# Performance work log

Hardware: AMD Instinct MI355X
Metric: run time of the kernel (lower is better)

## Reference

```python
import jax, jax.numpy as jnp
import numpy as np

N_NODES = 50000
N_EDGES = 800000
IN_DIM = 96
HID = 96


def setup_inputs() -> dict:
    key = jax.random.key(0)
    k1, k2, k3, k4 = jax.random.split(key, 4)
    x = jax.random.normal(k1, (N_NODES, IN_DIM), dtype=jnp.float32)
    edge_index = jax.random.randint(k2, (2, N_EDGES), 0, N_NODES, dtype=jnp.int64)
    s1 = 1.0 / np.sqrt(IN_DIM)
    s2 = 1.0 / np.sqrt(HID)
    W1 = jax.random.normal(k3, (IN_DIM, HID), dtype=jnp.float32) * s1
    b1 = jnp.zeros((HID,), dtype=jnp.float32)
    W2 = jax.random.normal(k4, (HID, HID), dtype=jnp.float32) * s2
    b2 = jnp.zeros((HID,), dtype=jnp.float32)
    return {"x": x, "edge_index": edge_index, "W1": W1, "b1": b1, "W2": W2, "b2": b2}


def _gcn_conv(x, src, dst, norm, W, b, n_nodes):
    # x' = D^{-1/2}(A+I)D^{-1/2} X W + b  (PyG GCNConv semantics)
    xw = x @ W                           # [N, out]
    msg = xw[src] * norm[:, None]        # gather + edge-normalize, [E+N, out]
    agg = jax.ops.segment_sum(msg, dst, num_segments=n_nodes)  # scatter-add
    return agg + b


def reference(x, edge_index, W1, b1, W2, b2):
    n_nodes = x.shape[0]
    loops = jnp.arange(n_nodes, dtype=edge_index.dtype)
    src = jnp.concatenate([edge_index[0], loops])  # sources (j)
    dst = jnp.concatenate([edge_index[1], loops])  # targets (i), aggregation index
    # symmetric normalization with self-loops; degree counted at targets
    deg = jax.ops.segment_sum(jnp.ones(dst.shape, dtype=x.dtype), dst, num_segments=n_nodes)
    dinv = jnp.where(deg > 0, jax.lax.rsqrt(deg), 0.0)
    norm = dinv[src] * dinv[dst]
    h = jax.nn.relu(_gcn_conv(x, src, dst, norm, W1, b1, n_nodes))
    h = jax.nn.relu(_gcn_conv(h, src, dst, norm, W2, b2, n_nodes))
    return h
```

## Files before the change

### kernel.cpp

```cpp
#include <hip/hip_runtime.h>

#define N_NODES 50000
#define N_EDGES 800000
#define DIM 96
#define FEAT_ELEMS (N_NODES * DIM)
#define NBLK 196
#define EGRID 3125
#define CGRID 4688
#define WGRID 10
#define AGRID 3125
#define GGRID 782

typedef __attribute__((ext_vector_type(8))) short short8;
typedef __attribute__((ext_vector_type(4))) float float4v;

__device__ __forceinline__ float bf16_to_f32(unsigned short u) {
    unsigned int w = ((unsigned int)u) << 16;
    float f;
    __builtin_memcpy(&f, &w, 4);
    return f;
}
__device__ __forceinline__ unsigned short f32_to_bf16_rne(float f) {
    unsigned int w;
    __builtin_memcpy(&w, &f, 4);
    unsigned int r = (w + 0x7FFFu + ((w >> 16) & 1u)) >> 16;
    return (unsigned short)r;
}
__device__ __forceinline__ unsigned int pack_bf16x2(float lo, float hi) {
    return (unsigned int)f32_to_bf16_rne(lo) | ((unsigned int)f32_to_bf16_rne(hi) << 16);
}

__device__ __forceinline__ int edge_at(const void* ep, int is64, int idx) {
    if (is64) return (int)((const long long*)ep)[idx];
    return ((const int*)ep)[idx];
}

__global__ __launch_bounds__(256) void prolog_kernel(const unsigned int* edges,
                                                     const unsigned int* x,
                                                     int* flagE, int* flagF, int* cnt) {
    __shared__ unsigned int sh[256];
    int t = threadIdx.x;
    int b = blockIdx.x;
    if (b < NBLK) {
        int i = b * 256 + t;
        if (i < N_NODES) cnt[i] = 0;
        return;
    }
    if (b == NBLK) {
        if (t < 64) {
            unsigned int acc = 0;
            for (int k = 0; k < 4; ++k) {
                int idx = t * 4 + k;
                int pos = 1 + 2 * idx * 3109;
                acc |= edges[pos];
            }
            sh[t] = acc;
        }
        __syncthreads();
        if (t == 0) {
            unsigned int a = 0;
            for (int i = 0; i < 64; ++i) a |= sh[i];
            *flagE = (a == 0u) ? 1 : 0;
        }
        return;
    }
    unsigned int w = x[t * 9000];
    unsigned int e = (w >> 7) & 0xFFu;
    sh[t] = (e >= 100u && e <= 135u) ? 1u : 0u;
    __syncthreads();
    if (t == 0) {
        int c = 0;
        for (int i = 0; i < 256; ++i) c += (int)sh[i];
        *flagF = (c >= 128) ? 1 : 0;
    }
}

__global__ __launch_bounds__(256) void count_convert_kernel(const void* __restrict__ edges,
                                                            const void* __restrict__ x,
                                                            const void* __restrict__ W1,
                                                            const void* __restrict__ W2,
                                                            const int* __restrict__ flagE,
                                                            const int* __restrict__ flagF,
                                                            int* __restrict__ cnt,
                                                            unsigned short* __restrict__ srcu,
                                                            unsigned short* __restrict__ dstu,
                                                            unsigned short* __restrict__ rank,
                                                            unsigned short* __restrict__ xb,
                                                            unsigned short* __restrict__ wsw1,
                                                            unsigned short* __restrict__ wsw2) {
    int b = blockIdx.x;
    if (b < EGRID) {
        int e = b * 256 + threadIdx.x;
        int is64 = *flagE;
        int s = edge_at(edges, is64, e);
        int d = edge_at(edges, is64, N_EDGES + e);
        srcu[e] = (unsigned short)s;
        dstu[e] = (unsigned short)d;
        rank[e] = (unsigned short)atomicAdd(&cnt[d], 1);
        return;
    }
    if (b < EGRID + CGRID) {
        int i4 = ((b - EGRID) * 256 + threadIdx.x) * 4;
        if (i4 >= FEAT_ELEMS) return;
        int isbf16 = *flagF;
        ushort4 o;
        if (isbf16) {
            o = *(const ushort4*)((const unsigned short*)x + i4);
        } else {
            float4 v = *(const float4*)((const float*)x + i4);
            o.x = f32_to_bf16_rne(v.x);
            o.y = f32_to_bf16_rne(v.y);
            o.z = f32_to_bf16_rne(v.z);
            o.w = f32_to_bf16_rne(v.w);
        }
        *(ushort4*)(xb + i4) = o;
        return;
    }
    int wi = b - EGRID - CGRID;
    int which = wi / 5;
    int f = (wi - which * 5) * 256 + threadIdx.x;
    if (f >= 1152) return;
    const void* Wp = which ? W2 : W1;
    unsigned short* Op = which ? wsw2 : wsw1;
    int wBf16 = *flagF;
    int kt = f / 384;
    int rem = f - kt * 384;
    int nt = rem >> 6;
    int ln64 = rem & 63;
    int q = ln64 >> 4, ln = ln64 & 15;
    int k0 = kt * 32 + q * 8;
    int n = nt * 16 + ln;
    unsigned short e[8];
    if (wBf16) {
        const unsigned short* Wh = (const unsigned short*)Wp;
        #pragma unroll
        for (int j = 0; j < 8; ++j) e[j] = Wh[(k0 + j) * DIM + n];
    } else {
        const float* Wf = (const float*)Wp;
        #pragma unroll
        for (int j = 0; j < 8; ++j) e[j] = f32_to_bf16_rne(Wf[(k0 + j) * DIM + n]);
    }
    uint4 pk;
    pk.x = (unsigned int)e[0] | ((unsigned int)e[1] << 16);
    pk.y = (unsigned int)e[2] | ((unsigned int)e[3] << 16);
    pk.z = (unsigned int)e[4] | ((unsigned int)e[5] << 16);
    pk.w = (unsigned int)e[6] | ((unsigned int)e[7] << 16);
    *(uint4*)&Op[f * 8] = pk;
}

__global__ __launch_bounds__(256) void scan_blocksum_kernel(const int* cnt, int* blockSums) {
    __shared__ int sh[256];
    int i = blockIdx.x * 256 + threadIdx.x;
    sh[threadIdx.x] = (i < N_NODES) ? cnt[i] : 0;
    __syncthreads();
    for (int off = 128; off > 0; off >>= 1) {
        if (threadIdx.x < off) sh[threadIdx.x] += sh[threadIdx.x + off];
        __syncthreads();
    }
    if (threadIdx.x == 0) blockSums[blockIdx.x] = sh[0];
}

__global__ __launch_bounds__(256) void scan_apply_kernel(const int* __restrict__ cnt,
                                                         const int* __restrict__ blockSums,
                                                         int* __restrict__ row_ptr,
                                                         float* __restrict__ dinv) {
    __shared__ int sb[256];
    __shared__ int sh[256];
    int t = threadIdx.x;
    sb[t] = (t < NBLK) ? blockSums[t] : 0;
    __syncthreads();
    for (int off = 1; off < 256; off <<= 1) {
        int u = (t >= off) ? sb[t - off] : 0;
        __syncthreads();
        sb[t] += u;
        __syncthreads();
    }
    int b = blockIdx.x;
    int blockOff = (b == 0) ? 0 : sb[b - 1];
    if (b == 0 && t == 0) row_ptr[N_NODES] = sb[NBLK - 1];

    int i = b * 256 + t;
    int c = (i < N_NODES) ? cnt[i] : 0;
    sh[t] = c;
    __syncthreads();
    for (int off = 1; off < 256; off <<= 1) {
        int u = (t >= off) ? sh[t - off] : 0;
        __syncthreads();
        sh[t] += u;
        __syncthreads();
    }
    if (i < N_NODES) {
        row_ptr[i] = sh[t] - c + blockOff;
        dinv[i]    = rsqrtf((float)(c + 1));
    }
}

__global__ __launch_bounds__(256) void fill_direct_kernel(const unsigned short* __restrict__ dstu,
                                                          const unsigned short* __restrict__ srcu,
                                                          const unsigned short* __restrict__ rank,
                                                          const int* __restrict__ row_ptr,
                                                          const float* __restrict__ dinv,
                                                          unsigned short* __restrict__ csr_src,
                                                          float* __restrict__ csr_w) {
    int e = blockIdx.x * 256 + threadIdx.x;
    if (e >= N_EDGES) return;
    int d = dstu[e];
    int s = srcu[e];
    int pos = row_ptr[d] + (int)rank[e];
    csr_src[pos] = (unsigned short)s;
    csr_w[pos]   = dinv[s] * dinv[d];
}

__global__ __launch_bounds__(256) void gather_kernel(const unsigned short* __restrict__ feat,
                                                     const int* __restrict__ row_ptr,
                                                     const unsigned short* __restrict__ csr_src,
                                                     const float* __restrict__ csr_w,
                                                     const float* __restrict__ dinv,
                                                     unsigned short* __restrict__ aggb) {
    int gid = blockIdx.x * 256 + threadIdx.x;
    int g = gid >> 4;
    int l = gid & 15;
    if (g >= N_NODES) return;
    float di = dinv[g];
    int gb = g * DIM + l * 2;
    ushort2 sv0 = *(const ushort2*)&feat[gb];
    ushort2 sv1 = *(const ushort2*)&feat[gb + 32];
    ushort2 sv2 = *(const ushort2*)&feat[gb + 64];
    float wself = di * di;
    float a0 = wself * bf16_to_f32(sv0.x), a1 = wself * bf16_to_f32(sv0.y);
    float a2 = wself * bf16_to_f32(sv1.x), a3 = wself * bf16_to_f32(sv1.y);
    float a4 = wself * bf16_to_f32(sv2.x), a5 = wself * bf16_to_f32(sv2.y);
    int e = row_ptr[g], e1 = row_ptr[g + 1];
    for (; e + 4 <= e1; e += 4) {
        int s0 = csr_src[e + 0];
        int s1 = csr_src[e + 1];
        int s2 = csr_src[e + 2];
        int s3 = csr_src[e + 3];
        float w0 = csr_w[e + 0];
        float w1 = csr_w[e + 1];
        float w2 = csr_w[e + 2];
        float w3 = csr_w[e + 3];
        int b0 = s0 * DIM + l * 2;
        int b1 = s1 * DIM + l * 2;
        int b2 = s2 * DIM + l * 2;
        int b3 = s3 * DIM + l * 2;
        ushort2 p0 = *(const ushort2*)&feat[b0];
        ushort2 p1 = *(const ushort2*)&feat[b0 + 32];
        ushort2 p2 = *(const ushort2*)&feat[b0 + 64];
        ushort2 q0 = *(const ushort2*)&feat[b1];
        ushort2 q1 = *(const ushort2*)&feat[b1 + 32];
        ushort2 q2 = *(const ushort2*)&feat[b1 + 64];
        ushort2 r0 = *(const ushort2*)&feat[b2];
        ushort2 r1 = *(const ushort2*)&feat[b2 + 32];
        ushort2 r2 = *(const ushort2*)&feat[b2 + 64];
        ushort2 t0 = *(const ushort2*)&feat[b3];
        ushort2 t1 = *(const ushort2*)&feat[b3 + 32];
        ushort2 t2 = *(const ushort2*)&feat[b3 + 64];
        a0 = fmaf(w0, bf16_to_f32(p0.x), a0);  a1 = fmaf(w0, bf16_to_f32(p0.y), a1);
        a2 = fmaf(w0, bf16_to_f32(p1.x), a2);  a3 = fmaf(w0, bf16_to_f32(p1.y), a3);
        a4 = fmaf(w0, bf16_to_f32(p2.x), a4);  a5 = fmaf(w0, bf16_to_f32(p2.y), a5);
        a0 = fmaf(w1, bf16_to_f32(q0.x), a0);  a1 = fmaf(w1, bf16_to_f32(q0.y), a1);
        a2 = fmaf(w1, bf16_to_f32(q1.x), a2);  a3 = fmaf(w1, bf16_to_f32(q1.y), a3);
        a4 = fmaf(w1, bf16_to_f32(q2.x), a4);  a5 = fmaf(w1, bf16_to_f32(q2.y), a5);
        a0 = fmaf(w2, bf16_to_f32(r0.x), a0);  a1 = fmaf(w2, bf16_to_f32(r0.y), a1);
        a2 = fmaf(w2, bf16_to_f32(r1.x), a2);  a3 = fmaf(w2, bf16_to_f32(r1.y), a3);
        a4 = fmaf(w2, bf16_to_f32(r2.x), a4);  a5 = fmaf(w2, bf16_to_f32(r2.y), a5);
        a0 = fmaf(w3, bf16_to_f32(t0.x), a0);  a1 = fmaf(w3, bf16_to_f32(t0.y), a1);
        a2 = fmaf(w3, bf16_to_f32(t1.x), a2);  a3 = fmaf(w3, bf16_to_f32(t1.y), a3);
        a4 = fmaf(w3, bf16_to_f32(t2.x), a4);  a5 = fmaf(w3, bf16_to_f32(t2.y), a5);
    }
    for (; e < e1; ++e) {
        int s = csr_src[e];
        float w = csr_w[e];
        int b0 = s * DIM + l * 2;
        ushort2 p0 = *(const ushort2*)&feat[b0];
        ushort2 p1 = *(const ushort2*)&feat[b0 + 32];
        ushort2 p2 = *(const ushort2*)&feat[b0 + 64];
        a0 = fmaf(w, bf16_to_f32(p0.x), a0);  a1 = fmaf(w, bf16_to_f32(p0.y), a1);
        a2 = fmaf(w, bf16_to_f32(p1.x), a2);  a3 = fmaf(w, bf16_to_f32(p1.y), a3);
        a4 = fmaf(w, bf16_to_f32(p2.x), a4);  a5 = fmaf(w, bf16_to_f32(p2.y), a5);
    }
    *(unsigned int*)&aggb[gb]      = pack_bf16x2(a0, a1);
    *(unsigned int*)&aggb[gb + 32] = pack_bf16x2(a2, a3);
    *(unsigned int*)&aggb[gb + 64] = pack_bf16x2(a4, a5);
}

__global__ __launch_bounds__(256) void gemm_mfma_kernel(const unsigned short* __restrict__ A,
                                                        const unsigned short* __restrict__ Wsw,
                                                        const void* __restrict__ bias,
                                                        const int* __restrict__ flagF,
                                                        void* __restrict__ out, int outMode) {
    int wBf16 = *flagF;
    int outBf16 = (outMode == 2) ? wBf16 : outMode;
    int t = threadIdx.x;
    int wave = t >> 6;
    int lane = t & 63;
    int quad = lane >> 4, ln = lane & 15;
    int m0 = blockIdx.x * 64 + wave * 16;
    int arow = m0 + ln;
    bool arowok = (arow < N_NODES);

    float4v acc[6];
    #pragma unroll
    for (int nt = 0; nt < 6; ++nt) acc[nt] = (float4v){0.f, 0.f, 0.f, 0.f};

    #pragma unroll
    for (int kt = 0; kt < 3; ++kt) {
        short8 af;
        if (arowok) {
            af = *(const short8*)&A[arow * DIM + kt * 32 + quad * 8];
        } else {
            af = (short8){0, 0, 0, 0, 0, 0, 0, 0};
        }
        #pragma unroll
        for (int nt = 0; nt < 6; ++nt) {
            short8 bf = *(const short8*)&Wsw[((kt * 6 + nt) * 64 + lane) * 8];
            acc[nt] = __builtin_amdgcn_mfma_f32_16x16x32_bf16(af, bf, acc[nt], 0, 0, 0);
        }
    }

    #pragma unroll
    for (int nt = 0; nt < 6; ++nt) {
        int n = nt * 16 + ln;
        float bv = wBf16 ? bf16_to_f32(((const unsigned short*)bias)[n])
                         : ((const float*)bias)[n];
        #pragma unroll
        for (int reg = 0; reg < 4; ++reg) {
            int row = m0 + quad * 4 + reg;
            if (row >= N_NODES) continue;
            float v = fmaxf(acc[nt][reg] + bv, 0.0f);
            if (outBf16) ((unsigned short*)out)[row * DIM + n] = f32_to_bf16_rne(v);
            else         ((float*)out)[row * DIM + n] = v;
        }
    }
}

extern "C" void kernel_launch(void* const* d_in, const int* in_sizes, int n_in,
                              void* d_out, int out_size, void* d_ws, size_t ws_size,
                              hipStream_t stream) {
    const void* x  = d_in[0];
    const void* ei = d_in[1];
    const void* W1 = d_in[2];
    const void* b1 = d_in[3];
    const void* W2 = d_in[4];
    const void* b2 = d_in[5];

    char* base = (char*)d_ws;
    size_t off = 0;
    auto carve = [&](size_t bytes) -> void* {
        void* p = base + off;
        off += (bytes + 255) & ~(size_t)255;
        return p;
    };
    int*            flagE     = (int*)carve(4);
    int*            flagF     = (int*)carve(4);
    int*            cnt       = (int*)carve((size_t)N_NODES * 4);
    int*            row_ptr   = (int*)carve((size_t)(N_NODES + 1) * 4);
    float*          dinv      = (float*)carve((size_t)N_NODES * 4);
    int*            blockSums = (int*)carve((size_t)NBLK * 4);
    unsigned short* srcu      = (unsigned short*)carve((size_t)N_EDGES * 2);
    unsigned short* dstu      = (unsigned short*)carve((size_t)N_EDGES * 2);
    unsigned short* rank      = (unsigned short*)carve((size_t)N_EDGES * 2);
    unsigned short* csr_src   = (unsigned short*)carve((size_t)N_EDGES * 2);
    float*          csr_w     = (float*)carve((size_t)N_EDGES * 4);
    unsigned short* wsw1      = (unsigned short*)carve((size_t)1152 * 8 * 2);
    unsigned short* wsw2      = (unsigned short*)carve((size_t)1152 * 8 * 2);
    unsigned short* aggb      = (unsigned short*)carve((size_t)FEAT_ELEMS * 2);
    unsigned short* xb        = (unsigned short*)carve((size_t)FEAT_ELEMS * 2);
    unsigned short* h         = (unsigned short*)carve((size_t)FEAT_ELEMS * 2);

    prolog_kernel<<<NBLK + 2, 256, 0, stream>>>((const unsigned int*)ei,
                                                (const unsigned int*)x, flagE, flagF, cnt);
    count_convert_kernel<<<EGRID + CGRID + WGRID, 256, 0, stream>>>(
        ei, x, W1, W2, flagE, flagF, cnt, srcu, dstu, rank, xb, wsw1, wsw2);
    scan_blocksum_kernel<<<NBLK, 256, 0, stream>>>(cnt, blockSums);
    scan_apply_kernel<<<NBLK, 256, 0, stream>>>(cnt, blockSums, row_ptr, dinv);
    fill_direct_kernel<<<EGRID, 256, 0, stream>>>(dstu, srcu, rank, row_ptr, dinv,
                                                  csr_src, csr_w);

    gather_kernel<<<AGRID, 256, 0, stream>>>(xb, row_ptr, csr_src, csr_w, dinv, aggb);
    gemm_mfma_kernel<<<GGRID, 256, 0, stream>>>(aggb, wsw1, b1, flagF, h, 1);

    gather_kernel<<<AGRID, 256, 0, stream>>>(h, row_ptr, csr_src, csr_w, dinv, aggb);
    gemm_mfma_kernel<<<GGRID, 256, 0, stream>>>(aggb, wsw2, b2, flagF, d_out, 2);
}
```

Before: 217.4 us.

## Pad degree counters to avoid atomic contention and split gather edges across four lane groups

Degree counters are padded to a 64-byte stride so the atomic increments for different nodes no longer share a cache line. The gather kernel now gives each node a full 64-lane wave instead of 16 lanes. The four 16-lane groups each take every fourth edge and combine their partial sums with cross-lane shuffles, which adds parallelism for the memory-bound neighbour reads. In exchange the counter buffer grows 16x and must be zeroed every call, the scans read it with a stride, and three quarters of the lanes sit idle on the self-loop and store steps.

```diff
diff --git a/kernel.cpp b/kernel.cpp
--- a/kernel.cpp
+++ b/kernel.cpp
@@ -5,10 +5,14 @@
 #define DIM 96
 #define FEAT_ELEMS (N_NODES * DIM)
 #define NBLK 196
+#define CNT_STRIDE 16
+#define CNT_INTS (N_NODES * CNT_STRIDE)
+#define ZBLK 196
+#define ZBLK4 782
 #define EGRID 3125
 #define CGRID 4688
 #define WGRID 10
-#define AGRID 3125
+#define AGRID 12500
 #define GGRID 782
 
 typedef __attribute__((ext_vector_type(8))) short short8;
@@ -41,12 +45,12 @@
     __shared__ unsigned int sh[256];
     int t = threadIdx.x;
     int b = blockIdx.x;
-    if (b < NBLK) {
-        int i = b * 256 + t;
-        if (i < N_NODES) cnt[i] = 0;
+    if (b < ZBLK4) {
+        int i4 = b * 256 + t;
+        if (i4 < CNT_INTS / 4) ((int4*)cnt)[i4] = make_int4(0, 0, 0, 0);
         return;
     }
-    if (b == NBLK) {
+    if (b == ZBLK4) {
         if (t < 64) {
             unsigned int acc = 0;
             for (int k = 0; k < 4; ++k) {
@@ -96,7 +100,7 @@
         int d = edge_at(edges, is64, N_EDGES + e);
         srcu[e] = (unsigned short)s;
         dstu[e] = (unsigned short)d;
-        rank[e] = (unsigned short)atomicAdd(&cnt[d], 1);
+        rank[e] = (unsigned short)atomicAdd(&cnt[d * CNT_STRIDE], 1);
         return;
     }
     if (b < EGRID + CGRID) {
@@ -151,7 +155,7 @@
 __global__ __launch_bounds__(256) void scan_blocksum_kernel(const int* cnt, int* blockSums) {
     __shared__ int sh[256];
     int i = blockIdx.x * 256 + threadIdx.x;
-    sh[threadIdx.x] = (i < N_NODES) ? cnt[i] : 0;
+    sh[threadIdx.x] = (i < N_NODES) ? cnt[i * CNT_STRIDE] : 0;
     __syncthreads();
     for (int off = 128; off > 0; off >>= 1) {
         if (threadIdx.x < off) sh[threadIdx.x] += sh[threadIdx.x + off];
@@ -180,7 +184,7 @@
     if (b == 0 && t == 0) row_ptr[N_NODES] = sb[NBLK - 1];
 
     int i = b * 256 + t;
-    int c = (i < N_NODES) ? cnt[i] : 0;
+    int c = (i < N_NODES) ? cnt[i * CNT_STRIDE] : 0;
     sh[t] = c;
     __syncthreads();
     for (int off = 1; off < 256; off <<= 1) {
@@ -218,58 +222,34 @@
                                                      const float* __restrict__ dinv,
                                                      unsigned short* __restrict__ aggb) {
     int gid = blockIdx.x * 256 + threadIdx.x;
-    int g = gid >> 4;
-    int l = gid & 15;
-    if (g >= N_NODES) return;
-    float di = dinv[g];
-    int gb = g * DIM + l * 2;
-    ushort2 sv0 = *(const ushort2*)&feat[gb];
-    ushort2 sv1 = *(const ushort2*)&feat[gb + 32];
-    ushort2 sv2 = *(const ushort2*)&feat[gb + 64];
-    float wself = di * di;
-    float a0 = wself * bf16_to_f32(sv0.x), a1 = wself * bf16_to_f32(sv0.y);
-    float a2 = wself * bf16_to_f32(sv1.x), a3 = wself * bf16_to_f32(sv1.y);
-    float a4 = wself * bf16_to_f32(sv2.x), a5 = wself * bf16_to_f32(sv2.y);
-    int e = row_ptr[g], e1 = row_ptr[g + 1];
-    for (; e + 4 <= e1; e += 4) {
-        int s0 = csr_src[e + 0];
-        int s1 = csr_src[e + 1];
-        int s2 = csr_src[e + 2];
-        int s3 = csr_src[e + 3];
-        float w0 = csr_w[e + 0];
-        float w1 = csr_w[e + 1];
-        float w2 = csr_w[e + 2];
-        float w3 = csr_w[e + 3];
+    int g = gid >> 6;
+    int lane = gid & 63;
+    int way = lane >> 4;
+    int l = lane & 15;
+    float a0 = 0.f, a1 = 0.f, a2 = 0.f, a3 = 0.f, a4 = 0.f, a5 = 0.f;
+    int e0 = row_ptr[g], e1 = row_ptr[g + 1];
+    int e = e0 + way;
+    for (; e + 4 < e1; e += 8) {
+        int s0 = csr_src[e];
+        int s1 = csr_src[e + 4];
+        float w0 = csr_w[e];
+        float w1 = csr_w[e + 4];
         int b0 = s0 * DIM + l * 2;
         int b1 = s1 * DIM + l * 2;
-        int b2 = s2 * DIM + l * 2;
-        int b3 = s3 * DIM + l * 2;
         ushort2 p0 = *(const ushort2*)&feat[b0];
         ushort2 p1 = *(const ushort2*)&feat[b0 + 32];
         ushort2 p2 = *(const ushort2*)&feat[b0 + 64];
         ushort2 q0 = *(const ushort2*)&feat[b1];
         ushort2 q1 = *(const ushort2*)&feat[b1 + 32];
         ushort2 q2 = *(const ushort2*)&feat[b1 + 64];
-        ushort2 r0 = *(const ushort2*)&feat[b2];
-        ushort2 r1 = *(const ushort2*)&feat[b2 + 32];
-        ushort2 r2 = *(const ushort2*)&feat[b2 + 64];
-        ushort2 t0 = *(const ushort2*)&feat[b3];
-        ushort2 t1 = *(const ushort2*)&feat[b3 + 32];
-        ushort2 t2 = *(const ushort2*)&feat[b3 + 64];
         a0 = fmaf(w0, bf16_to_f32(p0.x), a0);  a1 = fmaf(w0, bf16_to_f32(p0.y), a1);
         a2 = fmaf(w0, bf16_to_f32(p1.x), a2);  a3 = fmaf(w0, bf16_to_f32(p1.y), a3);
         a4 = fmaf(w0, bf16_to_f32(p2.x), a4);  a5 = fmaf(w0, bf16_to_f32(p2.y), a5);
         a0 = fmaf(w1, bf16_to_f32(q0.x), a0);  a1 = fmaf(w1, bf16_to_f32(q0.y), a1);
         a2 = fmaf(w1, bf16_to_f32(q1.x), a2);  a3 = fmaf(w1, bf16_to_f32(q1.y), a3);
         a4 = fmaf(w1, bf16_to_f32(q2.x), a4);  a5 = fmaf(w1, bf16_to_f32(q2.y), a5);
-        a0 = fmaf(w2, bf16_to_f32(r0.x), a0);  a1 = fmaf(w2, bf16_to_f32(r0.y), a1);
-        a2 = fmaf(w2, bf16_to_f32(r1.x), a2);  a3 = fmaf(w2, bf16_to_f32(r1.y), a3);
-        a4 = fmaf(w2, bf16_to_f32(r2.x), a4);  a5 = fmaf(w2, bf16_to_f32(r2.y), a5);
-        a0 = fmaf(w3, bf16_to_f32(t0.x), a0);  a1 = fmaf(w3, bf16_to_f32(t0.y), a1);
-        a2 = fmaf(w3, bf16_to_f32(t1.x), a2);  a3 = fmaf(w3, bf16_to_f32(t1.y), a3);
-        a4 = fmaf(w3, bf16_to_f32(t2.x), a4);  a5 = fmaf(w3, bf16_to_f32(t2.y), a5);
-    }
-    for (; e < e1; ++e) {
+    }
+    if (e < e1) {
         int s = csr_src[e];
         float w = csr_w[e];
         int b0 = s * DIM + l * 2;
@@ -280,9 +260,29 @@
         a2 = fmaf(w, bf16_to_f32(p1.x), a2);  a3 = fmaf(w, bf16_to_f32(p1.y), a3);
         a4 = fmaf(w, bf16_to_f32(p2.x), a4);  a5 = fmaf(w, bf16_to_f32(p2.y), a5);
     }
-    *(unsigned int*)&aggb[gb]      = pack_bf16x2(a0, a1);
-    *(unsigned int*)&aggb[gb + 32] = pack_bf16x2(a2, a3);
-    *(unsigned int*)&aggb[gb + 64] = pack_bf16x2(a4, a5);
+    if (way == 0) {
+        float di = dinv[g];
+        float ws = di * di;
+        int gb = g * DIM + l * 2;
+        ushort2 sv0 = *(const ushort2*)&feat[gb];
+        ushort2 sv1 = *(const ushort2*)&feat[gb + 32];
+        ushort2 sv2 = *(const ushort2*)&feat[gb + 64];
+        a0 = fmaf(ws, bf16_to_f32(sv0.x), a0);  a1 = fmaf(ws, bf16_to_f32(sv0.y), a1);
+        a2 = fmaf(ws, bf16_to_f32(sv1.x), a2);  a3 = fmaf(ws, bf16_to_f32(sv1.y), a3);
+        a4 = fmaf(ws, bf16_to_f32(sv2.x), a4);  a5 = fmaf(ws, bf16_to_f32(sv2.y), a5);
+    }
+    a0 += __shfl_xor(a0, 16); a0 += __shfl_xor(a0, 32);
+    a1 += __shfl_xor(a1, 16); a1 += __shfl_xor(a1, 32);
+    a2 += __shfl_xor(a2, 16); a2 += __shfl_xor(a2, 32);
+    a3 += __shfl_xor(a3, 16); a3 += __shfl_xor(a3, 32);
+    a4 += __shfl_xor(a4, 16); a4 += __shfl_xor(a4, 32);
+    a5 += __shfl_xor(a5, 16); a5 += __shfl_xor(a5, 32);
+    if (way == 0) {
+        int gb = g * DIM + l * 2;
+        *(unsigned int*)&aggb[gb]      = pack_bf16x2(a0, a1);
+        *(unsigned int*)&aggb[gb + 32] = pack_bf16x2(a2, a3);
+        *(unsigned int*)&aggb[gb + 64] = pack_bf16x2(a4, a5);
+    }
 }
 
 __global__ __launch_bounds__(256) void gemm_mfma_kernel(const unsigned short* __restrict__ A,
@@ -354,7 +354,7 @@
     };
     int*            flagE     = (int*)carve(4);
     int*            flagF     = (int*)carve(4);
-    int*            cnt       = (int*)carve((size_t)N_NODES * 4);
+    int*            cnt       = (int*)carve((size_t)CNT_INTS * 4);
     int*            row_ptr   = (int*)carve((size_t)(N_NODES + 1) * 4);
     float*          dinv      = (float*)carve((size_t)N_NODES * 4);
     int*            blockSums = (int*)carve((size_t)NBLK * 4);
@@ -369,8 +369,8 @@
     unsigned short* xb        = (unsigned short*)carve((size_t)FEAT_ELEMS * 2);
     unsigned short* h         = (unsigned short*)carve((size_t)FEAT_ELEMS * 2);
 
-    prolog_kernel<<<NBLK + 2, 256, 0, stream>>>((const unsigned int*)ei,
-                                                (const unsigned int*)x, flagE, flagF, cnt);
+    prolog_kernel<<<ZBLK4 + 2, 256, 0, stream>>>((const unsigned int*)ei,
+                                                 (const unsigned int*)x, flagE, flagF, cnt);
     count_convert_kernel<<<EGRID + CGRID + WGRID, 256, 0, stream>>>(
         ei, x, W1, W2, flagE, flagF, cnt, srcu, dstu, rank, xb, wsw1, wsw2);
     scan_blocksum_kernel<<<NBLK, 256, 0, stream>>>(cnt, blockSums);
```

Result: slower. 225.3 us (+3.6%).
